# Performance work log

Measured on AMD Instinct MI355X. Metric: run time of the kernel, lower is better.

Reference implementation:

```python
import jax, jax.numpy as jnp
import numpy as np

H = 512
S = 65  # 64 board cells + appended constant 1


def _heads(y, wk, wq, wv):
    # y: [H, S]; wk/wq/wv: [3, H, H] -> atts: [3, S, H]
    def one(wk_i, wq_i, wv_i):
        k = wk_i @ y            # [H, S]
        q = wq_i @ y            # [H, S]
        v = wv_i @ y            # [H, S]
        sm = jax.nn.softmax(k.T @ q, axis=1)  # [S, S], softmax over dim=1
        return sm @ v.T         # [S, H]
    return jax.vmap(one)(wk, wq, wv)


def setup_inputs() -> dict:
    key = jax.random.key(0)
    ks = jax.random.split(key, 10)
    r = lambda k, s: jax.random.normal(k, s, dtype=jnp.float32)
    return {
        "inputs": r(ks[0], (1, 64)),
        "embedding": r(ks[1], (H, S)),
        "wq": r(ks[2], (3, 3, H, H)),
        "wk": r(ks[3], (3, 3, H, H)),
        "wv": r(ks[4], (3, 3, H, H)),
        "linear1": r(ks[5], (3 * H, H)),
        "linear2": r(ks[6], (3 * H, H)),
        "linear3": r(ks[7], (3 * H, 2 * H)),
        "linear4": r(ks[8], (2 * H, H)),
        "linear5": r(ks[9], (H, 64)),
    }


def reference(inputs, embedding, wq, wk, wv, linear1, linear2, linear3, linear4, linear5):
    x = jnp.concatenate([inputs[0], jnp.ones((1,), inputs.dtype)])  # [S]
    y = embedding * x  # [H, S] (broadcast over rows)

    # Layer 1 (3 heads)
    a1 = _heads(y, wk[0], wq[0], wv[0])  # [3, S, H]
    y = jax.nn.relu(jnp.concatenate([a1[0], a1[1], a1[2]], axis=1) @ linear1).T  # [H, S]

    # Layer 2 -- NOTE: original code cats att11, att12, att23 (a bug we preserve)
    a2 = _heads(y, wk[1], wq[1], wv[1])
    y = jax.nn.relu(jnp.concatenate([a1[0], a1[1], a2[2]], axis=1) @ linear2).T  # [H, S]

    # Layer 3 -- NOTE: original code cats att11, att12, att33 (preserved)
    a3 = _heads(y, wk[2], wq[2], wv[2])
    y = jax.nn.relu(jnp.concatenate([a1[0], a1[1], a3[2]], axis=1) @ linear3)[64]  # [2H]

    # dropout p=0.1 -> identity in eval mode
    y = jnp.tanh(y @ linear4)  # [H]
    score = y @ linear5        # [64]
    return score[None, :]      # [1, 64]
```

## Files before the change

### kernel.cpp

```cpp
#include <hip/hip_runtime.h>
#include <hip/hip_bf16.h>
#include <math.h>

#define H 512
#define S 65
#define SP 80
#define HS (H * S)
#define PHS (H * SP)
#define KS3 24
#define KS4 16


__global__ void scale_embed_kernel(const float* __restrict__ inp,
                                   const float* __restrict__ emb,
                                   float* __restrict__ yT) {
    int i = blockIdx.x * blockDim.x + threadIdx.x;
    if (i < PHS) {
        int s = i / H;
        int h = i % H;
        float v = 0.0f;
        if (s < S) {
            float x = (s == 64) ? 1.0f : inp[s];
            v = emb[h * S + s] * x;
        }
        yT[i] = v;
    }
}

__global__ void __launch_bounds__(256, 2)
kqv_gemm_tiled(const float* __restrict__ wq,
               const float* __restrict__ wk,
               const float* __restrict__ wv,
               int layer, int head0,
               const float* __restrict__ yT,
               float* __restrict__ part) {
    int slot  = blockIdx.z;
    int which = blockIdx.y;
    int mat = layer * 3 + head0 + slot;
    const float* W = (which == 0 ? wk : (which == 1 ? wq : wv)) + (size_t)mat * H * H;

    int n0   = (blockIdx.x & 7) * 64;
    int kidx = blockIdx.x >> 3;

    __shared__ float Wt[64 * 64];
    __shared__ float As[SP * 64];

    int t  = threadIdx.x;
    int nq = t & 15;
    int g  = t >> 4;

    float4 acc[5];
#pragma unroll
    for (int r = 0; r < 5; ++r) acc[r] = make_float4(0.f, 0.f, 0.f, 0.f);

    for (int ch = 0; ch < 4; ++ch) {
        int kc0 = kidx * 256 + ch * 64;

#pragma unroll
        for (int c = 0; c < 4; ++c) {
            int f = c * 256 + t;
            int wn  = f >> 4;
            int kf4 = f & 15;
            float4 w4 = *(const float4*)(W + (size_t)(n0 + wn) * H + kc0 + 4 * kf4);
            int sw = ((wn >> 2) ^ (kf4 & 7));
            int base = (4 * kf4) * 64 + 4 * sw + (wn & 3);
            Wt[base      ] = w4.x;
            Wt[base +  64] = w4.y;
            Wt[base + 128] = w4.z;
            Wt[base + 192] = w4.w;
        }
#pragma unroll
        for (int c = 0; c < 5; ++c) {
            int f = c * 256 + t;
            int as  = f >> 4;
            int kf4 = f & 15;
            *(float4*)(&As[as * 64 + 4 * kf4]) =
                *(const float4*)(yT + (size_t)as * H + kc0 + 4 * kf4);
        }
        __syncthreads();

#pragma unroll
        for (int k4 = 0; k4 < 16; ++k4) {
            int swc = 4 * (nq ^ (k4 & 7));
            float4 w0 = *(const float4*)(&Wt[(4 * k4 + 0) * 64 + swc]);
            float4 w1 = *(const float4*)(&Wt[(4 * k4 + 1) * 64 + swc]);
            float4 w2 = *(const float4*)(&Wt[(4 * k4 + 2) * 64 + swc]);
            float4 w3 = *(const float4*)(&Wt[(4 * k4 + 3) * 64 + swc]);
#pragma unroll
            for (int r = 0; r < 5; ++r) {
                float4 a = *(const float4*)(&As[(g + 16 * r) * 64 + 4 * k4]);
                acc[r].x = fmaf(a.x, w0.x, acc[r].x);
                acc[r].y = fmaf(a.x, w0.y, acc[r].y);
                acc[r].z = fmaf(a.x, w0.z, acc[r].z);
                acc[r].w = fmaf(a.x, w0.w, acc[r].w);
                acc[r].x = fmaf(a.y, w1.x, acc[r].x);
                acc[r].y = fmaf(a.y, w1.y, acc[r].y);
                acc[r].z = fmaf(a.y, w1.z, acc[r].z);
                acc[r].w = fmaf(a.y, w1.w, acc[r].w);
                acc[r].x = fmaf(a.z, w2.x, acc[r].x);
                acc[r].y = fmaf(a.z, w2.y, acc[r].y);
                acc[r].z = fmaf(a.z, w2.z, acc[r].z);
                acc[r].w = fmaf(a.z, w2.w, acc[r].w);
                acc[r].x = fmaf(a.w, w3.x, acc[r].x);
                acc[r].y = fmaf(a.w, w3.y, acc[r].y);
                acc[r].z = fmaf(a.w, w3.z, acc[r].z);
                acc[r].w = fmaf(a.w, w3.w, acc[r].w);
            }
        }
        __syncthreads();
    }

    float* P = part + (size_t)((slot * 3 + which) * 2 + kidx) * PHS;
#pragma unroll
    for (int r = 0; r < 5; ++r) {
        *(float4*)(P + (size_t)(g + 16 * r) * H + n0 + 4 * nq) = acc[r];
    }
}

__global__ void attn_kernel(const float* __restrict__ kqvp,
                            float* __restrict__ att) {
    int a = blockIdx.x;
    int slot = blockIdx.y;
    int tid = threadIdx.x;

    const float* K0 = kqvp + (size_t)(slot * 3 + 0) * 2 * PHS;
    const float* K1 = K0 + PHS;
    const float* Q0 = kqvp + (size_t)(slot * 3 + 1) * 2 * PHS;
    const float* Q1 = Q0 + PHS;
    const float* V0 = kqvp + (size_t)(slot * 3 + 2) * 2 * PHS;
    const float* V1 = V0 + PHS;
    float* ao = att + (size_t)slot * S * H;

    __shared__ float ka[H];
    __shared__ float smv[S];
    __shared__ float p[S];

    ka[tid]       = K0[(size_t)a * H + tid]       + K1[(size_t)a * H + tid];
    ka[tid + 256] = K0[(size_t)a * H + tid + 256] + K1[(size_t)a * H + tid + 256];
    __syncthreads();

    if (tid < S) {
        const float4* q0 = (const float4*)(Q0 + (size_t)tid * H);
        const float4* q1 = (const float4*)(Q1 + (size_t)tid * H);
        const float4* kl = (const float4*)ka;
        float4 c0 = {0,0,0,0}, c1 = {0,0,0,0};
        for (int t = 0; t < H / 4; t += 2) {
            float4 qa = q0[t],     qb = q1[t];
            float4 qc = q0[t + 1], qd = q1[t + 1];
            float4 k0 = kl[t], k1 = kl[t + 1];
            c0.x = fmaf(k0.x, qa.x + qb.x, c0.x);
            c0.y = fmaf(k0.y, qa.y + qb.y, c0.y);
            c0.z = fmaf(k0.z, qa.z + qb.z, c0.z);
            c0.w = fmaf(k0.w, qa.w + qb.w, c0.w);
            c1.x = fmaf(k1.x, qc.x + qd.x, c1.x);
            c1.y = fmaf(k1.y, qc.y + qd.y, c1.y);
            c1.z = fmaf(k1.z, qc.z + qd.z, c1.z);
            c1.w = fmaf(k1.w, qc.w + qd.w, c1.w);
        }
        smv[tid] = ((c0.x + c0.y) + (c0.z + c0.w)) + ((c1.x + c1.y) + (c1.z + c1.w));
    }
    __syncthreads();

    float maxv = -INFINITY;
    for (int i = 0; i < S; ++i) maxv = fmaxf(maxv, smv[i]);
    float sum = 0.0f;
    for (int i = 0; i < S; ++i) sum += expf(smv[i] - maxv);
    float inv = 1.0f / sum;
    if (tid < S) p[tid] = expf(smv[tid] - maxv) * inv;
    __syncthreads();

#pragma unroll
    for (int rep = 0; rep < 2; ++rep) {
        int hh = tid + rep * 256;
        float a0 = 0.f, a1 = 0.f;
#pragma unroll 4
        for (int b = 0; b < 64; b += 2) {
            a0 = fmaf(p[b    ], V0[(size_t)(b    ) * H + hh] + V1[(size_t)(b    ) * H + hh], a0);
            a1 = fmaf(p[b + 1], V0[(size_t)(b + 1) * H + hh] + V1[(size_t)(b + 1) * H + hh], a1);
        }
        a0 = fmaf(p[64], V0[(size_t)64 * H + hh] + V1[(size_t)64 * H + hh], a0);
        ao[(size_t)a * H + hh] = a0 + a1;
    }
}

__global__ void linA_kernel(const float* __restrict__ att1,
                            const float* __restrict__ lin1,
                            const float* __restrict__ lin2,
                            float* __restrict__ part1,
                            float* __restrict__ part2) {
    int seg = blockIdx.y;
    int i = blockIdx.x * blockDim.x + threadIdx.x;
    int s = i / H;
    int h = i % H;

    const float* att;
    const float* L;
    float* dst;
    if (seg < 6) {
        att = att1 + (size_t)(seg >> 1) * HS;
        L   = lin1 + (size_t)(seg * 256) * H + h;
        dst = part1 + (size_t)seg * HS;
    } else {
        int s2 = seg - 6;
        att = att1 + (size_t)(s2 >> 1) * HS;
        L   = lin2 + (size_t)(s2 * 256) * H + h;
        dst = part2 + (size_t)s2 * HS;
    }
    const float* row = att + (size_t)s * H + (seg & 1) * 256;

    float a0 = 0.f, a1 = 0.f, a2 = 0.f, a3 = 0.f;
    for (int j = 0; j < 256; j += 4) {
        a0 = fmaf(row[j + 0], L[(size_t)(j + 0) * H], a0);
        a1 = fmaf(row[j + 1], L[(size_t)(j + 1) * H], a1);
        a2 = fmaf(row[j + 2], L[(size_t)(j + 2) * H], a2);
        a3 = fmaf(row[j + 3], L[(size_t)(j + 3) * H], a3);
    }
    dst[i] = (a0 + a1) + (a2 + a3);
}

__global__ void lin2c_kernel(const float* __restrict__ att2,
                             const float* __restrict__ lin2,
                             float* __restrict__ part2) {
    int seg = 4 + blockIdx.y;
    int i = blockIdx.x * blockDim.x + threadIdx.x;
    int s = i / H;
    int h = i % H;

    const float* row = att2 + (size_t)s * H + (seg & 1) * 256;
    const float* L = lin2 + (size_t)(seg * 256) * H + h;

    float a0 = 0.f, a1 = 0.f, a2 = 0.f, a3 = 0.f;
    for (int j = 0; j < 256; j += 4) {
        a0 = fmaf(row[j + 0], L[(size_t)(j + 0) * H], a0);
        a1 = fmaf(row[j + 1], L[(size_t)(j + 1) * H], a1);
        a2 = fmaf(row[j + 2], L[(size_t)(j + 2) * H], a2);
        a3 = fmaf(row[j + 3], L[(size_t)(j + 3) * H], a3);
    }
    part2[(size_t)seg * HS + i] = (a0 + a1) + (a2 + a3);
}

__global__ void combine_relu_kernel(const float* __restrict__ part,
                                    float* __restrict__ yT) {
    int i = blockIdx.x * blockDim.x + threadIdx.x;
    if (i >= HS) return;
    float s = part[i] + part[HS + i] + part[2 * HS + i]
            + part[3 * HS + i] + part[4 * HS + i] + part[5 * HS + i];
    yT[i] = fmaxf(s, 0.0f);
}

__global__ void lin3ab_kernel(const float* __restrict__ att1,
                              const float* __restrict__ lin3,
                              float* __restrict__ tpart) {
    int j2 = blockIdx.x * 256 + threadIdx.x;
    int ks = blockIdx.y;
    const float* row = att1 + (size_t)(ks >> 3) * HS + (size_t)64 * H;
    int j0 = (ks & 7) * 64;
    int jbase = ks * 64;

    float a0 = 0.f, a1 = 0.f, a2 = 0.f, a3 = 0.f;
    for (int j = 0; j < 64; j += 4) {
        a0 = fmaf(row[j0 + j + 0], lin3[(size_t)(jbase + j + 0) * 1024 + j2], a0);
        a1 = fmaf(row[j0 + j + 1], lin3[(size_t)(jbase + j + 1) * 1024 + j2], a1);
        a2 = fmaf(row[j0 + j + 2], lin3[(size_t)(jbase + j + 2) * 1024 + j2], a2);
        a3 = fmaf(row[j0 + j + 3], lin3[(size_t)(jbase + j + 3) * 1024 + j2], a3);
    }
    tpart[ks * 1024 + j2] = (a0 + a1) + (a2 + a3);
}

__global__ void attn3_lin3c_kernel(const float* __restrict__ kqvp,
                                   const float* __restrict__ lin3,
                                   float* __restrict__ tpart) {
    int tid = threadIdx.x;
    int ks  = 16 + blockIdx.y;
    int j2  = blockIdx.x * 256 + tid;
    int j0  = (ks & 7) * 64;

    const float* K0 = kqvp;
    const float* K1 = kqvp + PHS;
    const float* Q0 = kqvp + 2 * (size_t)PHS;
    const float* Q1 = kqvp + 3 * (size_t)PHS;
    const float* V0 = kqvp + 4 * (size_t)PHS;
    const float* V1 = kqvp + 5 * (size_t)PHS;

    __shared__ float ka[H];
    __shared__ float smv[S];
    __shared__ float p[S];
    __shared__ float att_s[64];

    ka[tid]       = K0[(size_t)64 * H + tid]       + K1[(size_t)64 * H + tid];
    ka[tid + 256] = K0[(size_t)64 * H + tid + 256] + K1[(size_t)64 * H + tid + 256];
    __syncthreads();

    if (tid < S) {
        const float4* q0 = (const float4*)(Q0 + (size_t)tid * H);
        const float4* q1 = (const float4*)(Q1 + (size_t)tid * H);
        const float4* kl = (const float4*)ka;
        float4 c0 = {0,0,0,0}, c1 = {0,0,0,0};
        for (int t = 0; t < H / 4; t += 2) {
            float4 qa = q0[t],     qb = q1[t];
            float4 qc = q0[t + 1], qd = q1[t + 1];
            float4 k0 = kl[t], k1 = kl[t + 1];
            c0.x = fmaf(k0.x, qa.x + qb.x, c0.x);
            c0.y = fmaf(k0.y, qa.y + qb.y, c0.y);
            c0.z = fmaf(k0.z, qa.z + qb.z, c0.z);
            c0.w = fmaf(k0.w, qa.w + qb.w, c0.w);
            c1.x = fmaf(k1.x, qc.x + qd.x, c1.x);
            c1.y = fmaf(k1.y, qc.y + qd.y, c1.y);
            c1.z = fmaf(k1.z, qc.z + qd.z, c1.z);
            c1.w = fmaf(k1.w, qc.w + qd.w, c1.w);
        }
        smv[tid] = ((c0.x + c0.y) + (c0.z + c0.w)) + ((c1.x + c1.y) + (c1.z + c1.w));
    }
    __syncthreads();

    float maxv = -INFINITY;
    for (int i = 0; i < S; ++i) maxv = fmaxf(maxv, smv[i]);
    float sum = 0.0f;
    for (int i = 0; i < S; ++i) sum += expf(smv[i] - maxv);
    float inv = 1.0f / sum;
    if (tid < S) p[tid] = expf(smv[tid] - maxv) * inv;
    __syncthreads();

    if (tid < 64) {
        int hh = j0 + tid;
        float a0 = 0.f, a1 = 0.f;
#pragma unroll 4
        for (int b = 0; b < 64; b += 2) {
            a0 = fmaf(p[b    ], V0[(size_t)(b    ) * H + hh] + V1[(size_t)(b    ) * H + hh], a0);
            a1 = fmaf(p[b + 1], V0[(size_t)(b + 1) * H + hh] + V1[(size_t)(b + 1) * H + hh], a1);
        }
        a0 = fmaf(p[64], V0[(size_t)64 * H + hh] + V1[(size_t)64 * H + hh], a0);
        att_s[tid] = a0 + a1;
    }
    __syncthreads();

    int jbase = ks * 64;
    float a0 = 0.f, a1 = 0.f, a2 = 0.f, a3 = 0.f;
    for (int j = 0; j < 64; j += 4) {
        a0 = fmaf(att_s[j + 0], lin3[(size_t)(jbase + j + 0) * 1024 + j2], a0);
        a1 = fmaf(att_s[j + 1], lin3[(size_t)(jbase + j + 1) * 1024 + j2], a1);
        a2 = fmaf(att_s[j + 2], lin3[(size_t)(jbase + j + 2) * 1024 + j2], a2);
        a3 = fmaf(att_s[j + 3], lin3[(size_t)(jbase + j + 3) * 1024 + j2], a3);
    }
    tpart[ks * 1024 + j2] = (a0 + a1) + (a2 + a3);
}

__global__ void lin4_partial_kernel(const float* __restrict__ tpart,
                                    const float* __restrict__ lin4,
                                    float* __restrict__ upart) {
    __shared__ float tl[64];
    int hh = blockIdx.x * 256 + threadIdx.x;
    int ks = blockIdx.y;
    int j2base = ks * 64;

    if (threadIdx.x < 64) {
        int j2 = j2base + threadIdx.x;
        float s = 0.f;
#pragma unroll
        for (int p = 0; p < KS3; ++p) s += tpart[p * 1024 + j2];
        tl[threadIdx.x] = fmaxf(s, 0.f);
    }
    __syncthreads();

    float a0 = 0.f, a1 = 0.f, a2 = 0.f, a3 = 0.f;
    for (int j = 0; j < 64; j += 4) {
        a0 = fmaf(tl[j + 0], lin4[(size_t)(j2base + j + 0) * H + hh], a0);
        a1 = fmaf(tl[j + 1], lin4[(size_t)(j2base + j + 1) * H + hh], a1);
        a2 = fmaf(tl[j + 2], lin4[(size_t)(j2base + j + 2) * H + hh], a2);
        a3 = fmaf(tl[j + 3], lin4[(size_t)(j2base + j + 3) * H + hh], a3);
    }
    upart[ks * H + hh] = (a0 + a1) + (a2 + a3);
}

__global__ void final_out_kernel(const float* __restrict__ upart,
                                 const float* __restrict__ lin5,
                                 float* __restrict__ out) {
    __shared__ float u[H];
    __shared__ float pr[8][64];
    int tid = threadIdx.x;

    {
        float s = 0.f;
#pragma unroll
        for (int p = 0; p < KS4; ++p) s += upart[p * H + tid];
        u[tid] = tanhf(s);
    }
    __syncthreads();

    int o  = tid & 63;
    int sl = tid >> 6;
    float acc = 0.f;
    int h0 = sl * 64;
#pragma unroll 8
    for (int j = 0; j < 64; ++j) {
        acc = fmaf(u[h0 + j], lin5[(h0 + j) * 64 + o], acc);
    }
    pr[sl][o] = acc;
    __syncthreads();

    if (tid < 64) {
        float s = 0.f;
#pragma unroll
        for (int p = 0; p < 8; ++p) s += pr[p][tid];
        out[tid] = s;
    }
}

extern "C" void kernel_launch(void* const* d_in, const int* in_sizes, int n_in,
                              void* d_out, int out_size, void* d_ws, size_t ws_size,
                              hipStream_t stream) {
    const float* inputs  = (const float*)d_in[0];
    const float* emb     = (const float*)d_in[1];
    const float* wq      = (const float*)d_in[2];
    const float* wk      = (const float*)d_in[3];
    const float* wv      = (const float*)d_in[4];
    const float* linear1 = (const float*)d_in[5];
    const float* linear2 = (const float*)d_in[6];
    const float* linear3 = (const float*)d_in[7];
    const float* linear4 = (const float*)d_in[8];
    const float* linear5 = (const float*)d_in[9];
    float* out = (float*)d_out;

    float* ws    = (float*)d_ws;
    float* y     = ws;
    float* kqvp  = y     + PHS;
    float* att1  = kqvp  + 18 * PHS;
    float* att2  = att1  + 3 * HS;
    float* part1 = att2  + HS;
    float* part2 = part1 + 6 * HS;
    float* tpart = part2 + 6 * HS;
    float* upart = tpart + KS3 * 1024;

    const int nb  = HS / 256;
    const int nbp = PHS / 256;

    scale_embed_kernel<<<nbp, 256, 0, stream>>>(inputs, emb, y);

    kqv_gemm_tiled<<<dim3(16, 3, 3), 256, 0, stream>>>(wq, wk, wv, 0, 0, y, kqvp);
    attn_kernel<<<dim3(S, 3), 256, 0, stream>>>(kqvp, att1);
    linA_kernel<<<dim3(nb, 10), 256, 0, stream>>>(att1, linear1, linear2, part1, part2);
    lin3ab_kernel<<<dim3(4, 16), 256, 0, stream>>>(att1, linear3, tpart);
    combine_relu_kernel<<<nb, 256, 0, stream>>>(part1, y);

    kqv_gemm_tiled<<<dim3(16, 3, 1), 256, 0, stream>>>(wq, wk, wv, 1, 2, y, kqvp);
    attn_kernel<<<dim3(S, 1), 256, 0, stream>>>(kqvp, att2);
    lin2c_kernel<<<dim3(nb, 2), 256, 0, stream>>>(att2, linear2, part2);
    combine_relu_kernel<<<nb, 256, 0, stream>>>(part2, y);

    kqv_gemm_tiled<<<dim3(16, 3, 1), 256, 0, stream>>>(wq, wk, wv, 2, 2, y, kqvp);
    attn3_lin3c_kernel<<<dim3(4, 8), 256, 0, stream>>>(kqvp, linear3, tpart);

    lin4_partial_kernel<<<dim3(2, KS4), 256, 0, stream>>>(tpart, linear4, upart);
    final_out_kernel<<<1, 512, 0, stream>>>(upart, linear5, out);
}
```

Measured before the change: 262.2 us.

## Fuse all stages into one cooperative persistent kernel with grid syncs

Replaces the chain of thirteen small kernel launches with a single cooperative kernel of 256 blocks that runs every stage and separates them with grid-wide barriers. The layer-2 lin2c and combine_relu steps are merged so the last two lin2 segments are computed inline during the ReLU combine. The goal is to remove per-launch overhead and the gaps between dependent kernels. In exchange each stage is capped at 256 blocks (lin1/lin2 runs as a grid-stride loop), occupancy is one block per CU, and every grid.sync has its own cost.

```diff
diff --git a/kernel.cpp b/kernel.cpp
--- a/kernel.cpp
+++ b/kernel.cpp
@@ -1,6 +1,9 @@
 #include <hip/hip_runtime.h>
 #include <hip/hip_bf16.h>
+#include <hip/hip_cooperative_groups.h>
 #include <math.h>
+
+namespace cg = cooperative_groups;
 
 #define H 512
 #define S 65
@@ -10,44 +13,16 @@
 #define KS3 24
 #define KS4 16
 
-
-__global__ void scale_embed_kernel(const float* __restrict__ inp,
-                                   const float* __restrict__ emb,
-                                   float* __restrict__ yT) {
-    int i = blockIdx.x * blockDim.x + threadIdx.x;
-    if (i < PHS) {
-        int s = i / H;
-        int h = i % H;
-        float v = 0.0f;
-        if (s < S) {
-            float x = (s == 64) ? 1.0f : inp[s];
-            v = emb[h * S + s] * x;
-        }
-        yT[i] = v;
-    }
-}
-
-__global__ void __launch_bounds__(256, 2)
-kqv_gemm_tiled(const float* __restrict__ wq,
-               const float* __restrict__ wk,
-               const float* __restrict__ wv,
-               int layer, int head0,
-               const float* __restrict__ yT,
-               float* __restrict__ part) {
-    int slot  = blockIdx.z;
-    int which = blockIdx.y;
-    int mat = layer * 3 + head0 + slot;
-    const float* W = (which == 0 ? wk : (which == 1 ? wq : wv)) + (size_t)mat * H * H;
-
-    int n0   = (blockIdx.x & 7) * 64;
-    int kidx = blockIdx.x >> 3;
-
-    __shared__ float Wt[64 * 64];
-    __shared__ float As[SP * 64];
-
-    int t  = threadIdx.x;
-    int nq = t & 15;
-    int g  = t >> 4;
+__device__ __forceinline__ void gemm_dev(const float* __restrict__ W,
+                                         const float* __restrict__ yT,
+                                         float* __restrict__ P,
+                                         int x, int tid,
+                                         float* __restrict__ Wt,
+                                         float* __restrict__ As) {
+    int n0   = (x & 7) * 64;
+    int kidx = x >> 3;
+    int nq = tid & 15;
+    int g  = tid >> 4;
 
     float4 acc[5];
 #pragma unroll
@@ -55,10 +30,9 @@
 
     for (int ch = 0; ch < 4; ++ch) {
         int kc0 = kidx * 256 + ch * 64;
-
 #pragma unroll
         for (int c = 0; c < 4; ++c) {
-            int f = c * 256 + t;
+            int f = c * 256 + tid;
             int wn  = f >> 4;
             int kf4 = f & 15;
             float4 w4 = *(const float4*)(W + (size_t)(n0 + wn) * H + kc0 + 4 * kf4);
@@ -71,7 +45,7 @@
         }
 #pragma unroll
         for (int c = 0; c < 5; ++c) {
-            int f = c * 256 + t;
+            int f = c * 256 + tid;
             int as  = f >> 4;
             int kf4 = f & 15;
             *(float4*)(&As[as * 64 + 4 * kf4]) =
@@ -110,30 +84,25 @@
         __syncthreads();
     }
 
-    float* P = part + (size_t)((slot * 3 + which) * 2 + kidx) * PHS;
 #pragma unroll
     for (int r = 0; r < 5; ++r) {
         *(float4*)(P + (size_t)(g + 16 * r) * H + n0 + 4 * nq) = acc[r];
     }
 }
 
-__global__ void attn_kernel(const float* __restrict__ kqvp,
-                            float* __restrict__ att) {
-    int a = blockIdx.x;
-    int slot = blockIdx.y;
-    int tid = threadIdx.x;
-
-    const float* K0 = kqvp + (size_t)(slot * 3 + 0) * 2 * PHS;
-    const float* K1 = K0 + PHS;
-    const float* Q0 = kqvp + (size_t)(slot * 3 + 1) * 2 * PHS;
-    const float* Q1 = Q0 + PHS;
-    const float* V0 = kqvp + (size_t)(slot * 3 + 2) * 2 * PHS;
-    const float* V1 = V0 + PHS;
-    float* ao = att + (size_t)slot * S * H;
-
-    __shared__ float ka[H];
-    __shared__ float smv[S];
-    __shared__ float p[S];
+__device__ __forceinline__ void attn_dev(const float* __restrict__ base,
+                                         float* __restrict__ aoRow,
+                                         int a, int tid,
+                                         float* __restrict__ sm) {
+    const float* K0 = base;
+    const float* K1 = base + PHS;
+    const float* Q0 = base + 2 * (size_t)PHS;
+    const float* Q1 = base + 3 * (size_t)PHS;
+    const float* V0 = base + 4 * (size_t)PHS;
+    const float* V1 = base + 5 * (size_t)PHS;
+    float* ka  = sm;
+    float* smv = sm + 512;
+    float* p   = sm + 580;
 
     ka[tid]       = K0[(size_t)a * H + tid]       + K1[(size_t)a * H + tid];
     ka[tid + 256] = K0[(size_t)a * H + tid + 256] + K1[(size_t)a * H + tid + 256];
@@ -179,230 +148,285 @@
             a1 = fmaf(p[b + 1], V0[(size_t)(b + 1) * H + hh] + V1[(size_t)(b + 1) * H + hh], a1);
         }
         a0 = fmaf(p[64], V0[(size_t)64 * H + hh] + V1[(size_t)64 * H + hh], a0);
-        ao[(size_t)a * H + hh] = a0 + a1;
-    }
+        aoRow[hh] = a0 + a1;
+    }
+    __syncthreads();
 }
 
-__global__ void linA_kernel(const float* __restrict__ att1,
-                            const float* __restrict__ lin1,
-                            const float* __restrict__ lin2,
-                            float* __restrict__ part1,
-                            float* __restrict__ part2) {
-    int seg = blockIdx.y;
-    int i = blockIdx.x * blockDim.x + threadIdx.x;
-    int s = i / H;
-    int h = i % H;
-
-    const float* att;
-    const float* L;
-    float* dst;
-    if (seg < 6) {
-        att = att1 + (size_t)(seg >> 1) * HS;
-        L   = lin1 + (size_t)(seg * 256) * H + h;
-        dst = part1 + (size_t)seg * HS;
-    } else {
-        int s2 = seg - 6;
-        att = att1 + (size_t)(s2 >> 1) * HS;
-        L   = lin2 + (size_t)(s2 * 256) * H + h;
-        dst = part2 + (size_t)s2 * HS;
-    }
-    const float* row = att + (size_t)s * H + (seg & 1) * 256;
-
-    float a0 = 0.f, a1 = 0.f, a2 = 0.f, a3 = 0.f;
-    for (int j = 0; j < 256; j += 4) {
-        a0 = fmaf(row[j + 0], L[(size_t)(j + 0) * H], a0);
-        a1 = fmaf(row[j + 1], L[(size_t)(j + 1) * H], a1);
-        a2 = fmaf(row[j + 2], L[(size_t)(j + 2) * H], a2);
-        a3 = fmaf(row[j + 3], L[(size_t)(j + 3) * H], a3);
-    }
-    dst[i] = (a0 + a1) + (a2 + a3);
-}
-
-__global__ void lin2c_kernel(const float* __restrict__ att2,
-                             const float* __restrict__ lin2,
-                             float* __restrict__ part2) {
-    int seg = 4 + blockIdx.y;
-    int i = blockIdx.x * blockDim.x + threadIdx.x;
-    int s = i / H;
-    int h = i % H;
-
-    const float* row = att2 + (size_t)s * H + (seg & 1) * 256;
-    const float* L = lin2 + (size_t)(seg * 256) * H + h;
-
-    float a0 = 0.f, a1 = 0.f, a2 = 0.f, a3 = 0.f;
-    for (int j = 0; j < 256; j += 4) {
-        a0 = fmaf(row[j + 0], L[(size_t)(j + 0) * H], a0);
-        a1 = fmaf(row[j + 1], L[(size_t)(j + 1) * H], a1);
-        a2 = fmaf(row[j + 2], L[(size_t)(j + 2) * H], a2);
-        a3 = fmaf(row[j + 3], L[(size_t)(j + 3) * H], a3);
-    }
-    part2[(size_t)seg * HS + i] = (a0 + a1) + (a2 + a3);
-}
-
-__global__ void combine_relu_kernel(const float* __restrict__ part,
-                                    float* __restrict__ yT) {
-    int i = blockIdx.x * blockDim.x + threadIdx.x;
-    if (i >= HS) return;
-    float s = part[i] + part[HS + i] + part[2 * HS + i]
-            + part[3 * HS + i] + part[4 * HS + i] + part[5 * HS + i];
-    yT[i] = fmaxf(s, 0.0f);
-}
-
-__global__ void lin3ab_kernel(const float* __restrict__ att1,
-                              const float* __restrict__ lin3,
-                              float* __restrict__ tpart) {
-    int j2 = blockIdx.x * 256 + threadIdx.x;
-    int ks = blockIdx.y;
-    const float* row = att1 + (size_t)(ks >> 3) * HS + (size_t)64 * H;
-    int j0 = (ks & 7) * 64;
-    int jbase = ks * 64;
-
-    float a0 = 0.f, a1 = 0.f, a2 = 0.f, a3 = 0.f;
-    for (int j = 0; j < 64; j += 4) {
-        a0 = fmaf(row[j0 + j + 0], lin3[(size_t)(jbase + j + 0) * 1024 + j2], a0);
-        a1 = fmaf(row[j0 + j + 1], lin3[(size_t)(jbase + j + 1) * 1024 + j2], a1);
-        a2 = fmaf(row[j0 + j + 2], lin3[(size_t)(jbase + j + 2) * 1024 + j2], a2);
-        a3 = fmaf(row[j0 + j + 3], lin3[(size_t)(jbase + j + 3) * 1024 + j2], a3);
-    }
-    tpart[ks * 1024 + j2] = (a0 + a1) + (a2 + a3);
-}
-
-__global__ void attn3_lin3c_kernel(const float* __restrict__ kqvp,
-                                   const float* __restrict__ lin3,
-                                   float* __restrict__ tpart) {
+__global__ void __launch_bounds__(256, 1)
+fused_model(const float* __restrict__ inputs, const float* __restrict__ emb,
+            const float* __restrict__ wq, const float* __restrict__ wk,
+            const float* __restrict__ wv,
+            const float* __restrict__ lin1, const float* __restrict__ lin2,
+            const float* __restrict__ lin3, const float* __restrict__ lin4,
+            const float* __restrict__ lin5, float* __restrict__ out,
+            float* __restrict__ yT, float* __restrict__ kqvp,
+            float* __restrict__ att1, float* __restrict__ att2,
+            float* __restrict__ part1, float* __restrict__ part2,
+            float* __restrict__ tpart, float* __restrict__ upart) {
+    cg::grid_group grid = cg::this_grid();
+    __shared__ __align__(16) float smem[9216];
+    float* Wt = smem;
+    float* As = smem + 4096;
     int tid = threadIdx.x;
-    int ks  = 16 + blockIdx.y;
-    int j2  = blockIdx.x * 256 + tid;
-    int j0  = (ks & 7) * 64;
-
-    const float* K0 = kqvp;
-    const float* K1 = kqvp + PHS;
-    const float* Q0 = kqvp + 2 * (size_t)PHS;
-    const float* Q1 = kqvp + 3 * (size_t)PHS;
-    const float* V0 = kqvp + 4 * (size_t)PHS;
-    const float* V1 = kqvp + 5 * (size_t)PHS;
-
-    __shared__ float ka[H];
-    __shared__ float smv[S];
-    __shared__ float p[S];
-    __shared__ float att_s[64];
-
-    ka[tid]       = K0[(size_t)64 * H + tid]       + K1[(size_t)64 * H + tid];
-    ka[tid + 256] = K0[(size_t)64 * H + tid + 256] + K1[(size_t)64 * H + tid + 256];
-    __syncthreads();
-
-    if (tid < S) {
-        const float4* q0 = (const float4*)(Q0 + (size_t)tid * H);
-        const float4* q1 = (const float4*)(Q1 + (size_t)tid * H);
-        const float4* kl = (const float4*)ka;
-        float4 c0 = {0,0,0,0}, c1 = {0,0,0,0};
-        for (int t = 0; t < H / 4; t += 2) {
-            float4 qa = q0[t],     qb = q1[t];
-            float4 qc = q0[t + 1], qd = q1[t + 1];
-            float4 k0 = kl[t], k1 = kl[t + 1];
-            c0.x = fmaf(k0.x, qa.x + qb.x, c0.x);
-            c0.y = fmaf(k0.y, qa.y + qb.y, c0.y);
-            c0.z = fmaf(k0.z, qa.z + qb.z, c0.z);
-            c0.w = fmaf(k0.w, qa.w + qb.w, c0.w);
-            c1.x = fmaf(k1.x, qc.x + qd.x, c1.x);
-            c1.y = fmaf(k1.y, qc.y + qd.y, c1.y);
-            c1.z = fmaf(k1.z, qc.z + qd.z, c1.z);
-            c1.w = fmaf(k1.w, qc.w + qd.w, c1.w);
-        }
-        smv[tid] = ((c0.x + c0.y) + (c0.z + c0.w)) + ((c1.x + c1.y) + (c1.z + c1.w));
-    }
-    __syncthreads();
-
-    float maxv = -INFINITY;
-    for (int i = 0; i < S; ++i) maxv = fmaxf(maxv, smv[i]);
-    float sum = 0.0f;
-    for (int i = 0; i < S; ++i) sum += expf(smv[i] - maxv);
-    float inv = 1.0f / sum;
-    if (tid < S) p[tid] = expf(smv[tid] - maxv) * inv;
-    __syncthreads();
-
-    if (tid < 64) {
-        int hh = j0 + tid;
-        float a0 = 0.f, a1 = 0.f;
+    int bid = blockIdx.x;
+
+    if (bid < 160) {
+        int i = bid * 256 + tid;
+        int s = i / H, h = i % H;
+        float v = 0.f;
+        if (s < S) {
+            float x = (s == 64) ? 1.0f : inputs[s];
+            v = emb[h * S + s] * x;
+        }
+        yT[i] = v;
+    }
+    grid.sync();
+
+    if (bid < 144) {
+        int x = bid & 15, r = bid >> 4;
+        int which = r % 3, slot = r / 3;
+        const float* W = (which == 0 ? wk : (which == 1 ? wq : wv)) + (size_t)slot * H * H;
+        float* P = kqvp + (size_t)((slot * 3 + which) * 2 + (x >> 3)) * PHS;
+        gemm_dev(W, yT, P, x, tid, Wt, As);
+    }
+    grid.sync();
+
+    if (bid < 195) {
+        int slot = bid / 65, a = bid % 65;
+        attn_dev(kqvp + (size_t)slot * 6 * PHS,
+                 att1 + (size_t)slot * HS + (size_t)a * H, a, tid, smem);
+    }
+    grid.sync();
+
+    for (int vb = bid; vb < 1364; vb += 256) {
+        if (vb < 1300) {
+            int x = vb % 130, seg = vb / 130;
+            int i = x * 256 + tid;
+            int s = i / H, h = i % H;
+            const float* att;
+            const float* L;
+            float* dst;
+            if (seg < 6) {
+                att = att1 + (size_t)(seg >> 1) * HS;
+                L   = lin1 + (size_t)(seg * 256) * H + h;
+                dst = part1 + (size_t)seg * HS;
+            } else {
+                int s2 = seg - 6;
+                att = att1 + (size_t)(s2 >> 1) * HS;
+                L   = lin2 + (size_t)(s2 * 256) * H + h;
+                dst = part2 + (size_t)s2 * HS;
+            }
+            const float* row = att + (size_t)s * H + (seg & 1) * 256;
+            float a0 = 0.f, a1 = 0.f, a2 = 0.f, a3 = 0.f;
+            for (int j = 0; j < 256; j += 4) {
+                a0 = fmaf(row[j + 0], L[(size_t)(j + 0) * H], a0);
+                a1 = fmaf(row[j + 1], L[(size_t)(j + 1) * H], a1);
+                a2 = fmaf(row[j + 2], L[(size_t)(j + 2) * H], a2);
+                a3 = fmaf(row[j + 3], L[(size_t)(j + 3) * H], a3);
+            }
+            dst[i] = (a0 + a1) + (a2 + a3);
+        } else {
+            int idx = vb - 1300;
+            int j2 = (idx & 3) * 256 + tid;
+            int ks = idx >> 2;
+            const float* row = att1 + (size_t)(ks >> 3) * HS + (size_t)64 * H;
+            int j0 = (ks & 7) * 64;
+            int jbase = ks * 64;
+            float a0 = 0.f, a1 = 0.f, a2 = 0.f, a3 = 0.f;
+            for (int j = 0; j < 64; j += 4) {
+                a0 = fmaf(row[j0 + j + 0], lin3[(size_t)(jbase + j + 0) * 1024 + j2], a0);
+                a1 = fmaf(row[j0 + j + 1], lin3[(size_t)(jbase + j + 1) * 1024 + j2], a1);
+                a2 = fmaf(row[j0 + j + 2], lin3[(size_t)(jbase + j + 2) * 1024 + j2], a2);
+                a3 = fmaf(row[j0 + j + 3], lin3[(size_t)(jbase + j + 3) * 1024 + j2], a3);
+            }
+            tpart[ks * 1024 + j2] = (a0 + a1) + (a2 + a3);
+        }
+    }
+    grid.sync();
+
+    if (bid < 130) {
+        int i = bid * 256 + tid;
+        float s = part1[i] + part1[HS + i] + part1[2 * HS + i]
+                + part1[3 * HS + i] + part1[4 * HS + i] + part1[5 * HS + i];
+        yT[i] = fmaxf(s, 0.0f);
+    }
+    grid.sync();
+
+    if (bid < 48) {
+        int x = bid & 15, which = bid >> 4;
+        const float* W = (which == 0 ? wk : (which == 1 ? wq : wv)) + (size_t)5 * H * H;
+        float* P = kqvp + (size_t)(which * 2 + (x >> 3)) * PHS;
+        gemm_dev(W, yT, P, x, tid, Wt, As);
+    }
+    grid.sync();
+
+    if (bid < 65) {
+        attn_dev(kqvp, att2 + (size_t)bid * H, bid, tid, smem);
+    }
+    grid.sync();
+
+    if (bid < 130) {
+        int i = bid * 256 + tid;
+        int s = i / H, h = i % H;
+        const float* row = att2 + (size_t)s * H;
+        const float* L4 = lin2 + (size_t)1024 * H + h;
+        const float* L5 = lin2 + (size_t)1280 * H + h;
+        float a0 = 0.f, a1 = 0.f, a2 = 0.f, a3 = 0.f;
+        for (int j = 0; j < 256; j += 4) {
+            a0 = fmaf(row[j + 0], L4[(size_t)(j + 0) * H], a0);
+            a1 = fmaf(row[j + 1], L4[(size_t)(j + 1) * H], a1);
+            a2 = fmaf(row[j + 2], L4[(size_t)(j + 2) * H], a2);
+            a3 = fmaf(row[j + 3], L4[(size_t)(j + 3) * H], a3);
+        }
+        float s4 = (a0 + a1) + (a2 + a3);
+        a0 = a1 = a2 = a3 = 0.f;
+        for (int j = 0; j < 256; j += 4) {
+            a0 = fmaf(row[256 + j + 0], L5[(size_t)(j + 0) * H], a0);
+            a1 = fmaf(row[256 + j + 1], L5[(size_t)(j + 1) * H], a1);
+            a2 = fmaf(row[256 + j + 2], L5[(size_t)(j + 2) * H], a2);
+            a3 = fmaf(row[256 + j + 3], L5[(size_t)(j + 3) * H], a3);
+        }
+        float s5 = (a0 + a1) + (a2 + a3);
+        float tot = part2[i] + part2[HS + i] + part2[2 * HS + i] + part2[3 * HS + i] + s4 + s5;
+        yT[i] = fmaxf(tot, 0.0f);
+    }
+    grid.sync();
+
+    if (bid < 48) {
+        int x = bid & 15, which = bid >> 4;
+        const float* W = (which == 0 ? wk : (which == 1 ? wq : wv)) + (size_t)8 * H * H;
+        float* P = kqvp + (size_t)(which * 2 + (x >> 3)) * PHS;
+        gemm_dev(W, yT, P, x, tid, Wt, As);
+    }
+    grid.sync();
+
+    if (bid < 32) {
+        int jx = bid & 3;
+        int ks = 16 + (bid >> 2);
+        int j2 = jx * 256 + tid;
+        int j0 = (ks & 7) * 64;
+        const float* K0 = kqvp;
+        const float* K1 = kqvp + PHS;
+        const float* Q0 = kqvp + 2 * (size_t)PHS;
+        const float* Q1 = kqvp + 3 * (size_t)PHS;
+        const float* V0 = kqvp + 4 * (size_t)PHS;
+        const float* V1 = kqvp + 5 * (size_t)PHS;
+        float* ka    = smem;
+        float* smv   = smem + 512;
+        float* p     = smem + 580;
+        float* att_s = smem + 648;
+
+        ka[tid]       = K0[(size_t)64 * H + tid]       + K1[(size_t)64 * H + tid];
+        ka[tid + 256] = K0[(size_t)64 * H + tid + 256] + K1[(size_t)64 * H + tid + 256];
+        __syncthreads();
+
+        if (tid < S) {
+            const float4* q0 = (const float4*)(Q0 + (size_t)tid * H);
+            const float4* q1 = (const float4*)(Q1 + (size_t)tid * H);
+            const float4* kl = (const float4*)ka;
+            float4 c0 = {0,0,0,0}, c1 = {0,0,0,0};
+            for (int t = 0; t < H / 4; t += 2) {
+                float4 qa = q0[t],     qb = q1[t];
+                float4 qc = q0[t + 1], qd = q1[t + 1];
+                float4 k0 = kl[t], k1 = kl[t + 1];
+                c0.x = fmaf(k0.x, qa.x + qb.x, c0.x);
+                c0.y = fmaf(k0.y, qa.y + qb.y, c0.y);
+                c0.z = fmaf(k0.z, qa.z + qb.z, c0.z);
+                c0.w = fmaf(k0.w, qa.w + qb.w, c0.w);
+                c1.x = fmaf(k1.x, qc.x + qd.x, c1.x);
+                c1.y = fmaf(k1.y, qc.y + qd.y, c1.y);
+                c1.z = fmaf(k1.z, qc.z + qd.z, c1.z);
+                c1.w = fmaf(k1.w, qc.w + qd.w, c1.w);
+            }
+            smv[tid] = ((c0.x + c0.y) + (c0.z + c0.w)) + ((c1.x + c1.y) + (c1.z + c1.w));
+        }
+        __syncthreads();
+
+        float maxv = -INFINITY;
+        for (int i = 0; i < S; ++i) maxv = fmaxf(maxv, smv[i]);
+        float sum = 0.0f;
+        for (int i = 0; i < S; ++i) sum += expf(smv[i] - maxv);
+        float inv = 1.0f / sum;
+        if (tid < S) p[tid] = expf(smv[tid] - maxv) * inv;
+        __syncthreads();
+
+        if (tid < 64) {
+            int hh = j0 + tid;
+            float a0 = 0.f, a1 = 0.f;
 #pragma unroll 4
-        for (int b = 0; b < 64; b += 2) {
-            a0 = fmaf(p[b    ], V0[(size_t)(b    ) * H + hh] + V1[(size_t)(b    ) * H + hh], a0);
-            a1 = fmaf(p[b + 1], V0[(size_t)(b + 1) * H + hh] + V1[(size_t)(b + 1) * H + hh], a1);
-        }
-        a0 = fmaf(p[64], V0[(size_t)64 * H + hh] + V1[(size_t)64 * H + hh], a0);
-        att_s[tid] = a0 + a1;
-    }
-    __syncthreads();
-
-    int jbase = ks * 64;
-    float a0 = 0.f, a1 = 0.f, a2 = 0.f, a3 = 0.f;
-    for (int j = 0; j < 64; j += 4) {
-        a0 = fmaf(att_s[j + 0], lin3[(size_t)(jbase + j + 0) * 1024 + j2], a0);
-        a1 = fmaf(att_s[j + 1], lin3[(size_t)(jbase + j + 1) * 1024 + j2], a1);
-        a2 = fmaf(att_s[j + 2], lin3[(size_t)(jbase + j + 2) * 1024 + j2], a2);
-        a3 = fmaf(att_s[j + 3], lin3[(size_t)(jbase + j + 3) * 1024 + j2], a3);
-    }
-    tpart[ks * 1024 + j2] = (a0 + a1) + (a2 + a3);
-}
-
-__global__ void lin4_partial_kernel(const float* __restrict__ tpart,
-                                    const float* __restrict__ lin4,
-                                    float* __restrict__ upart) {
-    __shared__ float tl[64];
-    int hh = blockIdx.x * 256 + threadIdx.x;
-    int ks = blockIdx.y;
-    int j2base = ks * 64;
-
-    if (threadIdx.x < 64) {
-        int j2 = j2base + threadIdx.x;
-        float s = 0.f;
-#pragma unroll
-        for (int p = 0; p < KS3; ++p) s += tpart[p * 1024 + j2];
-        tl[threadIdx.x] = fmaxf(s, 0.f);
-    }
-    __syncthreads();
-
-    float a0 = 0.f, a1 = 0.f, a2 = 0.f, a3 = 0.f;
-    for (int j = 0; j < 64; j += 4) {
-        a0 = fmaf(tl[j + 0], lin4[(size_t)(j2base + j + 0) * H + hh], a0);
-        a1 = fmaf(tl[j + 1], lin4[(size_t)(j2base + j + 1) * H + hh], a1);
-        a2 = fmaf(tl[j + 2], lin4[(size_t)(j2base + j + 2) * H + hh], a2);
-        a3 = fmaf(tl[j + 3], lin4[(size_t)(j2base + j + 3) * H + hh], a3);
-    }
-    upart[ks * H + hh] = (a0 + a1) + (a2 + a3);
-}
-
-__global__ void final_out_kernel(const float* __restrict__ upart,
-                                 const float* __restrict__ lin5,
-                                 float* __restrict__ out) {
-    __shared__ float u[H];
-    __shared__ float pr[8][64];
-    int tid = threadIdx.x;
-
-    {
-        float s = 0.f;
-#pragma unroll
-        for (int p = 0; p < KS4; ++p) s += upart[p * H + tid];
-        u[tid] = tanhf(s);
-    }
-    __syncthreads();
-
-    int o  = tid & 63;
-    int sl = tid >> 6;
-    float acc = 0.f;
-    int h0 = sl * 64;
+            for (int b = 0; b < 64; b += 2) {
+                a0 = fmaf(p[b    ], V0[(size_t)(b    ) * H + hh] + V1[(size_t)(b    ) * H + hh], a0);
+                a1 = fmaf(p[b + 1], V0[(size_t)(b + 1) * H + hh] + V1[(size_t)(b + 1) * H + hh], a1);
+            }
+            a0 = fmaf(p[64], V0[(size_t)64 * H + hh] + V1[(size_t)64 * H + hh], a0);
+            att_s[tid] = a0 + a1;
+        }
+        __syncthreads();
+
+        int jbase = ks * 64;
+        float a0 = 0.f, a1 = 0.f, a2 = 0.f, a3 = 0.f;
+        for (int j = 0; j < 64; j += 4) {
+            a0 = fmaf(att_s[j + 0], lin3[(size_t)(jbase + j + 0) * 1024 + j2], a0);
+            a1 = fmaf(att_s[j + 1], lin3[(size_t)(jbase + j + 1) * 1024 + j2], a1);
+            a2 = fmaf(att_s[j + 2], lin3[(size_t)(jbase + j + 2) * 1024 + j2], a2);
+            a3 = fmaf(att_s[j + 3], lin3[(size_t)(jbase + j + 3) * 1024 + j2], a3);
+        }
+        tpart[ks * 1024 + j2] = (a0 + a1) + (a2 + a3);
+    }
+    grid.sync();
+
+    if (bid < 32) {
+        float* tl = smem;
+        int hh = (bid & 1) * 256 + tid;
+        int ks = bid >> 1;
+        int j2base = ks * 64;
+        if (tid < 64) {
+            int j2 = j2base + tid;
+            float s = 0.f;
+#pragma unroll
+            for (int p = 0; p < KS3; ++p) s += tpart[p * 1024 + j2];
+            tl[tid] = fmaxf(s, 0.f);
+        }
+        __syncthreads();
+        float a0 = 0.f, a1 = 0.f, a2 = 0.f, a3 = 0.f;
+        for (int j = 0; j < 64; j += 4) {
+            a0 = fmaf(tl[j + 0], lin4[(size_t)(j2base + j + 0) * H + hh], a0);
+            a1 = fmaf(tl[j + 1], lin4[(size_t)(j2base + j + 1) * H + hh], a1);
+            a2 = fmaf(tl[j + 2], lin4[(size_t)(j2base + j + 2) * H + hh], a2);
+            a3 = fmaf(tl[j + 3], lin4[(size_t)(j2base + j + 3) * H + hh], a3);
+        }
+        upart[ks * H + hh] = (a0 + a1) + (a2 + a3);
+    }
+    grid.sync();
+
+    if (bid == 0) {
+        float* u  = smem;
+        float* pr = smem + 512;
+        float s0 = 0.f, s1 = 0.f;
+#pragma unroll
+        for (int p = 0; p < KS4; ++p) {
+            s0 += upart[p * H + tid];
+            s1 += upart[p * H + tid + 256];
+        }
+        u[tid]       = tanhf(s0);
+        u[tid + 256] = tanhf(s1);
+        __syncthreads();
+
+        int o  = tid & 63;
+        int sl = tid >> 6;
+        float acc = 0.f;
+        int h0 = sl * 128;
 #pragma unroll 8
-    for (int j = 0; j < 64; ++j) {
-        acc = fmaf(u[h0 + j], lin5[(h0 + j) * 64 + o], acc);
-    }
-    pr[sl][o] = acc;
-    __syncthreads();
-
-    if (tid < 64) {
-        float s = 0.f;
-#pragma unroll
-        for (int p = 0; p < 8; ++p) s += pr[p][tid];
-        out[tid] = s;
+        for (int j = 0; j < 128; ++j) {
+            acc = fmaf(u[h0 + j], lin5[(h0 + j) * 64 + o], acc);
+        }
+        pr[sl * 64 + o] = acc;
+        __syncthreads();
+
+        if (tid < 64) {
+            out[tid] = ((pr[tid] + pr[64 + tid]) + (pr[128 + tid] + pr[192 + tid]));
+        }
     }
 }
 
@@ -428,28 +452,17 @@
     float* att2  = att1  + 3 * HS;
     float* part1 = att2  + HS;
     float* part2 = part1 + 6 * HS;
-    float* tpart = part2 + 6 * HS;
+    float* tpart = part2 + 4 * HS;
     float* upart = tpart + KS3 * 1024;
 
-    const int nb  = HS / 256;
-    const int nbp = PHS / 256;
-
-    scale_embed_kernel<<<nbp, 256, 0, stream>>>(inputs, emb, y);
-
-    kqv_gemm_tiled<<<dim3(16, 3, 3), 256, 0, stream>>>(wq, wk, wv, 0, 0, y, kqvp);
-    attn_kernel<<<dim3(S, 3), 256, 0, stream>>>(kqvp, att1);
-    linA_kernel<<<dim3(nb, 10), 256, 0, stream>>>(att1, linear1, linear2, part1, part2);
-    lin3ab_kernel<<<dim3(4, 16), 256, 0, stream>>>(att1, linear3, tpart);
-    combine_relu_kernel<<<nb, 256, 0, stream>>>(part1, y);
-
-    kqv_gemm_tiled<<<dim3(16, 3, 1), 256, 0, stream>>>(wq, wk, wv, 1, 2, y, kqvp);
-    attn_kernel<<<dim3(S, 1), 256, 0, stream>>>(kqvp, att2);
-    lin2c_kernel<<<dim3(nb, 2), 256, 0, stream>>>(att2, linear2, part2);
-    combine_relu_kernel<<<nb, 256, 0, stream>>>(part2, y);
-
-    kqv_gemm_tiled<<<dim3(16, 3, 1), 256, 0, stream>>>(wq, wk, wv, 2, 2, y, kqvp);
-    attn3_lin3c_kernel<<<dim3(4, 8), 256, 0, stream>>>(kqvp, linear3, tpart);
-
-    lin4_partial_kernel<<<dim3(2, KS4), 256, 0, stream>>>(tpart, linear4, upart);
-    final_out_kernel<<<1, 512, 0, stream>>>(upart, linear5, out);
+    void* args[] = {
+        (void*)&inputs, (void*)&emb, (void*)&wq, (void*)&wk, (void*)&wv,
+        (void*)&linear1, (void*)&linear2, (void*)&linear3, (void*)&linear4,
+        (void*)&linear5, (void*)&out,
+        (void*)&y, (void*)&kqvp, (void*)&att1, (void*)&att2,
+        (void*)&part1, (void*)&part2, (void*)&tpart, (void*)&upart
+    };
+
+    hipLaunchCooperativeKernel((void*)fused_model, dim3(256), dim3(256),
+                               args, 0, stream);
 }
```

Measured after the change: 562.6 us. 115% more time.
